# Performance work log

Measured on AMD Instinct MI355X. Metric: run time of the kernel, lower is better.

## Reference

```python
import jax, jax.numpy as jnp
import numpy as np

B, C, H, W = 16, 512, 64, 64
NH, HD = 8, 64  # num_heads, head_dim; C == NH*HD
EPS_ATTN = 1e-5
EPS_BN = 1e-5


def setup_inputs() -> dict:
    key = jax.random.key(0)
    k = jax.random.split(key, 9)
    x = jax.random.normal(k[0], (B, C, H, W), dtype=jnp.float32)
    # grouped 1x1 conv qkv: groups=NH, in/group=HD, out/group=3*HD
    w1 = jax.random.normal(k[1], (NH, 3 * HD, HD), dtype=jnp.float32) * 0.05
    b1 = jax.random.normal(k[2], (NH, 3 * HD), dtype=jnp.float32) * 0.01
    # grouped 1x1 conv qkv2: groups=HD, in/group=NH, out/group=3*NH
    w2 = jax.random.normal(k[3], (HD, 3 * NH, NH), dtype=jnp.float32) * 0.05
    b2 = jax.random.normal(k[4], (HD, 3 * NH), dtype=jnp.float32) * 0.01
    gamma = 1.0 + 0.1 * jax.random.normal(k[5], (C,), dtype=jnp.float32)
    beta = 0.1 * jax.random.normal(k[6], (C,), dtype=jnp.float32)
    rmean = 0.1 * jax.random.normal(k[7], (C,), dtype=jnp.float32)
    rvar = 0.5 + jax.random.uniform(k[8], (C,), dtype=jnp.float32)
    return {"x": x, "w1": w1, "b1": b1, "w2": w2, "b2": b2,
            "gamma": gamma, "beta": beta, "rmean": rmean, "rvar": rvar}


def _signed_sqrt_softmax(a):
    a = jnp.sign(a) * jnp.sqrt(jnp.abs(a) + EPS_ATTN)
    return jax.nn.softmax(a, axis=-1)


def reference(x, w1, b1, w2, b2, gamma, beta, rmean, rvar):
    N = H * W
    # ---- stage 1: grouped 1x1 conv (groups=NH) ----
    xg = x.reshape(B, NH, HD, N)
    qkv = jnp.einsum('goi,bgin->bgon', w1, xg) + b1[None, :, :, None]  # [B,NH,3HD,N]
    # torch grouped-conv channel order is group-major -> flatten then split as in source
    q, k, v = jnp.moveaxis(qkv.reshape(B, 3 * C, N).reshape(B, 3, NH, HD, N), 1, 0)
    attn = jnp.einsum('bhdn,bhen->bhde', q, k) * (HD ** -0.5)  # [B,NH,HD,HD]
    attn = _signed_sqrt_softmax(attn)
    out = jnp.einsum('bhde,bhen->bhdn', attn, v)  # [B,NH,HD,N]
    x1 = out.reshape(B, C, H, W) + x
    x1 = jnp.transpose(x1.reshape(B, NH, HD, H, W), (0, 2, 1, 3, 4)).reshape(B, C, H, W)
    # ---- BatchNorm2d (eval mode) + ReLU ----
    inv = gamma / jnp.sqrt(rvar + EPS_BN)
    y = x1 * inv[None, :, None, None] + (beta - rmean * inv)[None, :, None, None]
    xr = jnp.maximum(y, 0.0)
    # ---- stage 2: grouped 1x1 conv (groups=HD) ----
    xg2 = xr.reshape(B, HD, NH, N)
    qkv2 = jnp.einsum('goi,bgin->bgon', w2, xg2) + b2[None, :, :, None]  # [B,HD,3NH,N]
    q2, k2, v2 = jnp.moveaxis(qkv2.reshape(B, 3 * C, N).reshape(B, 3, HD, NH, N), 1, 0)
    attn2 = jnp.einsum('bdhn,bden->bdhe', q2, k2) * (NH ** -0.5)  # [B,HD,NH,NH]
    attn2 = _signed_sqrt_softmax(attn2)
    out2 = jnp.einsum('bdhe,bden->bdhn', attn2, v2)  # [B,HD,NH,N]
    x2 = jnp.transpose(out2.reshape(B, HD, NH, H, W), (0, 2, 1, 3, 4)).reshape(B, C, H, W) + y
    return x2
```

## Files before the change

### kernel.cpp

```cpp
#include <hip/hip_runtime.h>

#define N_ 4096

typedef __attribute__((ext_vector_type(8))) short bf16x8;
typedef __attribute__((ext_vector_type(4))) short bf16x4;
typedef __attribute__((ext_vector_type(4))) float f32x4;

__device__ __forceinline__ float ssqrt(float a) {
  if (a == 0.f) return 0.f;
  return copysignf(sqrtf(fabsf(a) + 1e-5f), a);
}

__device__ __forceinline__ ushort f2bf(float f) {
  uint u = __float_as_uint(f);
  u += 0x7fff + ((u >> 16) & 1);
  return (ushort)(u >> 16);
}
__device__ __forceinline__ float bf2f(ushort h) {
  return __uint_as_float((uint)h << 16);
}

__device__ __forceinline__ void split2(float f, ushort& hi, ushort& lo) {
  uint u = __float_as_uint(f);
  hi = (ushort)(u >> 16);
  float lof = f - __uint_as_float(u & 0xffff0000u);
  lo = (ushort)(__float_as_uint(lof) >> 16);
}

__device__ __forceinline__ f32x4 mfma16(bf16x8 a, bf16x8 b, f32x4 c) {
  return __builtin_amdgcn_mfma_f32_16x16x32_bf16(a, b, c, 0, 0, 0);
}

__device__ __forceinline__ bf16x8 relu8(bf16x8 v) {
  union { bf16x8 h; uint u[4]; } x;
  x.h = v;
#pragma unroll
  for (int i = 0; i < 4; ++i) {
    uint m = x.u[i] & 0x80008000u;
    x.u[i] &= ~((m >> 15) * 0xFFFFu);
  }
  return x.h;
}

__device__ __forceinline__ bf16x8 ld8_b64(const ushort* p) {
  bf16x4 a = *(const bf16x4*)p;
  bf16x4 b = *(const bf16x4*)(p + 4);
  return (bf16x8){a[0], a[1], a[2], a[3], b[0], b[1], b[2], b[3]};
}

__global__ __launch_bounds__(256) void k1_gram(const float* __restrict__ x,
    float* __restrict__ Gp, float* __restrict__ sums) {
  const int GQ[6] = {0, 0, 1, 1, 2, 2};
  const int GK[6] = {2, 3, 3, 4, 4, 5};
  int bid = (blockIdx.x & 7) * 48 + (blockIdx.x >> 3);
  int s = bid / 96, rem = bid % 96;
  int b = rem / 6, pid = rem % 6;
  int gq = GQ[pid], gk = GK[pid];
  const float* A = x + ((size_t)b * 512 + gq * 64) * N_ + s * 1024;
  const float* B = x + ((size_t)b * 512 + gk * 64) * N_ + s * 1024;
  __shared__ __attribute__((aligned(16))) ushort Ah[64][72], Al[64][72];
  __shared__ __attribute__((aligned(16))) ushort Bh[64][72], Bl[64][72];
  int t = threadIdx.x;
  int lr = t >> 2, lq = t & 3;
  int l = t & 63, w = t >> 6;
  int mw = (w >> 1) * 32, nw = (w & 1) * 32;
  int fr = l & 15, ko = (l >> 4) * 8;
  float sumA = 0.f, sumB = 0.f;
  f32x4 acc[2][2];
#pragma unroll
  for (int i = 0; i < 2; ++i)
#pragma unroll
    for (int j = 0; j < 2; ++j) acc[i][j] = (f32x4){0.f, 0.f, 0.f, 0.f};

  for (int kt = 0; kt < 16; ++kt) {
    int kbase = kt * 64 + lq * 16;
#pragma unroll
    for (int j = 0; j < 4; ++j) {
      float4 va = *(const float4*)(A + (size_t)lr * N_ + kbase + j * 4);
      float4 vb = *(const float4*)(B + (size_t)lr * N_ + kbase + j * 4);
      sumA += va.x + va.y + va.z + va.w;
      sumB += vb.x + vb.y + vb.z + vb.w;
      ushort4 ha, la, hb, lb;
      split2(va.x, ha.x, la.x); split2(va.y, ha.y, la.y);
      split2(va.z, ha.z, la.z); split2(va.w, ha.w, la.w);
      split2(vb.x, hb.x, lb.x); split2(vb.y, hb.y, lb.y);
      split2(vb.z, hb.z, lb.z); split2(vb.w, hb.w, lb.w);
      int c0 = lq * 16 + j * 4;
      *(ushort4*)&Ah[lr][c0] = ha;
      *(ushort4*)&Al[lr][c0] = la;
      *(ushort4*)&Bh[lr][c0] = hb;
      *(ushort4*)&Bl[lr][c0] = lb;
    }
    __syncthreads();
#pragma unroll
    for (int wk = 0; wk < 2; ++wk) {
      int kk = wk * 32 + ko;
      bf16x8 ah[2], al[2], bh[2], bl[2];
#pragma unroll
      for (int mt = 0; mt < 2; ++mt) {
        ah[mt] = *(const bf16x8*)&Ah[mw + mt * 16 + fr][kk];
        al[mt] = *(const bf16x8*)&Al[mw + mt * 16 + fr][kk];
      }
#pragma unroll
      for (int nt = 0; nt < 2; ++nt) {
        bh[nt] = *(const bf16x8*)&Bh[nw + nt * 16 + fr][kk];
        bl[nt] = *(const bf16x8*)&Bl[nw + nt * 16 + fr][kk];
      }
#pragma unroll
      for (int mt = 0; mt < 2; ++mt)
#pragma unroll
        for (int nt = 0; nt < 2; ++nt) {
          acc[mt][nt] = mfma16(ah[mt], bh[nt], acc[mt][nt]);
          acc[mt][nt] = mfma16(ah[mt], bl[nt], acc[mt][nt]);
          acc[mt][nt] = mfma16(al[mt], bh[nt], acc[mt][nt]);
        }
    }
    __syncthreads();
  }
  size_t base = ((size_t)s * 96 + rem) * 4096;
#pragma unroll
  for (int mt = 0; mt < 2; ++mt)
#pragma unroll
    for (int nt = 0; nt < 2; ++nt)
#pragma unroll
      for (int reg = 0; reg < 4; ++reg) {
        int gr = mw + mt * 16 + (l >> 4) * 4 + reg;
        int gc = nw + nt * 16 + fr;
        Gp[base + (size_t)gr * 64 + gc] = acc[mt][nt][reg];
      }
  sumA += __shfl_xor(sumA, 1); sumA += __shfl_xor(sumA, 2);
  sumB += __shfl_xor(sumB, 1); sumB += __shfl_xor(sumB, 2);
  if (lq == 0) {
    sums[(((size_t)s * 16 + b) * 6 + gq) * 64 + lr] = sumA;
    sums[(((size_t)s * 16 + b) * 6 + gk) * 64 + lr] = sumB;
  }
}

__global__ __launch_bounds__(256) void k2_attn1(
    const float* __restrict__ w1, const float* __restrict__ b1,
    const float* __restrict__ Gp, const float* __restrict__ sums,
    ushort* __restrict__ M1h, ushort* __restrict__ M1l,
    float* __restrict__ pbv1) {
  const int PID[8] = {0, 1, 1, 2, 3, 3, 4, 5};
  int bh = blockIdx.x;
  int b = bh >> 3, h = bh & 7;
  int pid = PID[h];
  int mq = h, mk = 8 + h, mv = 16 + h;
  int gq = mq / 3, oq0 = (mq % 3) * 64;
  int gk = mk / 3, ok0 = (mk % 3) * 64;
  int gv = mv / 3, ov0 = (mv % 3) * 64;
  __shared__ __attribute__((aligned(16))) float Gs[64][68];
  __shared__ __attribute__((aligned(16))) float Was[64][68];
  __shared__ __attribute__((aligned(16))) float Wbs[64][68];
  __shared__ __attribute__((aligned(16))) float Ts[64][68];
  __shared__ float sxs[64], sks[64], vqs[64], vks[64], bvs[64];
  int t = threadIdx.x, tx = t & 15, ty = t >> 4;
  int d0 = ty * 4, e0 = tx * 4;

  for (int f = t; f < 4096; f += 256) {
    int dd = f >> 6, ee = f & 63;
    float g = 0.f;
#pragma unroll
    for (int s = 0; s < 4; ++s)
      g += Gp[((size_t)s * 96 + b * 6 + pid) * 4096 + f];
    Gs[dd][ee] = g;
    Was[dd][ee] = w1[((size_t)(gq * 192 + oq0 + dd)) * 64 + ee];
    Wbs[dd][ee] = w1[((size_t)(gk * 192 + ok0 + dd)) * 64 + ee];
  }
  if (t < 64) {
    float v = 0.f, w = 0.f;
#pragma unroll
    for (int s = 0; s < 4; ++s) {
      v += sums[(((size_t)s * 16 + b) * 6 + gq) * 64 + t];
      w += sums[(((size_t)s * 16 + b) * 6 + gk) * 64 + t];
    }
    sxs[t] = v; sks[t] = w;
    bvs[t] = b1[gv * 192 + ov0 + t];
  }
  __syncthreads();
  if (t < 64) {
    float vq = 0.f, vk = 0.f;
    for (int i = 0; i < 64; ++i) { vq += Was[t][i] * sxs[i]; vk += Wbs[t][i] * sks[i]; }
    vqs[t] = vq; vks[t] = vk;
  }
  {
    float acc[4][4] = {};
    for (int i = 0; i < 64; i += 4) {
      float4 a4[4], g4[4];
#pragma unroll
      for (int r = 0; r < 4; ++r) a4[r] = *(const float4*)&Was[d0 + r][i];
#pragma unroll
      for (int k = 0; k < 4; ++k) g4[k] = *(const float4*)&Gs[i + k][e0];
#pragma unroll
      for (int r = 0; r < 4; ++r) {
        const float* ap = (const float*)&a4[r];
#pragma unroll
        for (int k = 0; k < 4; ++k) {
          const float* gp = (const float*)&g4[k];
#pragma unroll
          for (int c = 0; c < 4; ++c) acc[r][c] += ap[k] * gp[c];
        }
      }
    }
#pragma unroll
    for (int r = 0; r < 4; ++r)
#pragma unroll
      for (int c = 0; c < 4; ++c) Ts[d0 + r][e0 + c] = acc[r][c];
  }
  __syncthreads();
  float P[4][4];
  {
    float s[4][4] = {};
    for (int j = 0; j < 64; j += 4) {
      float4 t4[4], w4[4];
#pragma unroll
      for (int r = 0; r < 4; ++r) t4[r] = *(const float4*)&Ts[d0 + r][j];
#pragma unroll
      for (int c = 0; c < 4; ++c) w4[c] = *(const float4*)&Wbs[e0 + c][j];
#pragma unroll
      for (int r = 0; r < 4; ++r)
#pragma unroll
        for (int c = 0; c < 4; ++c)
          s[r][c] += t4[r].x * w4[c].x + t4[r].y * w4[c].y
                   + t4[r].z * w4[c].z + t4[r].w * w4[c].w;
    }
    float bq_[4], bk_[4];
#pragma unroll
    for (int r = 0; r < 4; ++r) bq_[r] = b1[gq * 192 + oq0 + d0 + r];
#pragma unroll
    for (int c = 0; c < 4; ++c) bk_[c] = b1[gk * 192 + ok0 + e0 + c];
#pragma unroll
    for (int r = 0; r < 4; ++r)
#pragma unroll
      for (int c = 0; c < 4; ++c) {
        float v = (s[r][c] + bq_[r] * vks[e0 + c] + bk_[c] * vqs[d0 + r]
                   + 4096.f * bq_[r] * bk_[c]) * 0.125f;
        s[r][c] = ssqrt(v);
      }
#pragma unroll
    for (int r = 0; r < 4; ++r) {
      float m = fmaxf(fmaxf(s[r][0], s[r][1]), fmaxf(s[r][2], s[r][3]));
#pragma unroll
      for (int mm = 1; mm < 16; mm <<= 1) m = fmaxf(m, __shfl_xor(m, mm));
      float sum = 0.f;
#pragma unroll
      for (int c = 0; c < 4; ++c) { s[r][c] = expf(s[r][c] - m); sum += s[r][c]; }
#pragma unroll
      for (int mm = 1; mm < 16; mm <<= 1) sum += __shfl_xor(sum, mm);
      float inv = 1.f / sum;
#pragma unroll
      for (int c = 0; c < 4; ++c) P[r][c] = s[r][c] * inv;
    }
  }
#pragma unroll
  for (int r = 0; r < 4; ++r)
#pragma unroll
    for (int c = 0; c < 4; ++c) Gs[d0 + r][e0 + c] = P[r][c];
  for (int f = t; f < 4096; f += 256) {
    int ee = f >> 6, ii = f & 63;
    Was[ee][ii] = w1[((size_t)(gv * 192 + ov0 + ee)) * 64 + ii];
  }
  __syncthreads();
  {
    float acc[4][4] = {};
    for (int e = 0; e < 64; e += 4) {
      float4 p4[4], v4[4];
#pragma unroll
      for (int r = 0; r < 4; ++r) p4[r] = *(const float4*)&Gs[d0 + r][e];
#pragma unroll
      for (int k = 0; k < 4; ++k) v4[k] = *(const float4*)&Was[e + k][e0];
#pragma unroll
      for (int r = 0; r < 4; ++r) {
        const float* pp = (const float*)&p4[r];
#pragma unroll
        for (int k = 0; k < 4; ++k) {
          const float* vp = (const float*)&v4[k];
#pragma unroll
          for (int c = 0; c < 4; ++c) acc[r][c] += pp[k] * vp[c];
        }
      }
    }
    ushort* MoH = M1h + (size_t)bh * 4096;
    ushort* MoL = M1l + (size_t)bh * 4096;
#pragma unroll
    for (int r = 0; r < 4; ++r)
#pragma unroll
      for (int c = 0; c < 4; ++c) {
        float vv = acc[r][c];
        ushort hi = f2bf(vv);
        MoH[(size_t)(d0 + r) * 64 + e0 + c] = hi;
        MoL[(size_t)(d0 + r) * 64 + e0 + c] = f2bf(vv - bf2f(hi));
      }
  }
  if (t < 64) {
    float pb = 0.f;
    for (int e = 0; e < 64; ++e) pb += Gs[t][e] * bvs[e];
    pbv1[(size_t)bh * 64 + t] = pb;
  }
}

__global__ __launch_bounds__(256) void k3_out1(const float* __restrict__ x,
    const ushort* __restrict__ M1h, const ushort* __restrict__ M1l,
    const float* __restrict__ pbv1,
    const float* __restrict__ gamma, const float* __restrict__ beta,
    const float* __restrict__ rmean, const float* __restrict__ rvar,
    ushort* __restrict__ y) {
  int orig = (blockIdx.x & 7) * 256 + (blockIdx.x >> 3);
  int b = orig >> 7;
  int rem = orig & 127;
  int chunk = rem >> 3, h = rem & 7;
  int bh = b * 8 + h;
  int gv = (16 + h) / 3;
  const float* Xv = x + ((size_t)b * 512 + gv * 64) * N_ + chunk * 256;
  const float* Xr = x + ((size_t)b * 512 + h * 64) * N_ + chunk * 256;
  ushort* Y = y + (size_t)b * 512 * N_ + chunk * 256;

  __shared__ __attribute__((aligned(16))) ushort Xth[64][68], Xtl[64][68];
  __shared__ float pbs[64], invs[64], adds[64];
  int t = threadIdx.x;
  if (t < 64) {
    pbs[t] = pbv1[(size_t)bh * 64 + t];
    int c = t * 8 + h;
    float iv = gamma[c] / sqrtf(rvar[c] + 1e-5f);
    invs[t] = iv;
    adds[t] = beta[c] - rmean[c] * iv;
  }
  int l = t & 63, w = t >> 6;
  int dq = w >> 1, nq = w & 1;
  int fr = l & 15, g = l >> 4;

  bf16x8 mh[2][2], ml[2][2];
  {
    const ushort* MbH = M1h + (size_t)bh * 4096;
    const ushort* MbL = M1l + (size_t)bh * 4096;
#pragma unroll
    for (int dr = 0; dr < 2; ++dr)
#pragma unroll
      for (int wk = 0; wk < 2; ++wk) {
        int off = (dq * 32 + dr * 16 + fr) * 64 + wk * 32 + g * 8;
        mh[dr][wk] = *(const bf16x8*)(MbH + off);
        ml[dr][wk] = *(const bf16x8*)(MbL + off);
      }
  }

  int e2 = t >> 3, q = t & 7;
  for (int tile = 0; tile < 4; ++tile) {
    int nb = tile * 64;
    {
      const float* r0p = Xv + (size_t)(2 * e2) * N_ + nb + q * 8;
      const float* r1p = r0p + N_;
      float4 a0 = *(const float4*)r0p, a1 = *(const float4*)(r0p + 4);
      float4 b0 = *(const float4*)r1p, b1 = *(const float4*)(r1p + 4);
      float ra[8] = {a0.x, a0.y, a0.z, a0.w, a1.x, a1.y, a1.z, a1.w};
      float rb[8] = {b0.x, b0.y, b0.z, b0.w, b1.x, b1.y, b1.z, b1.w};
#pragma unroll
      for (int i = 0; i < 8; ++i) {
        int n = q * 8 + i;
        ushort h0, l0, h1, l1;
        split2(ra[i], h0, l0);
        split2(rb[i], h1, l1);
        *(uint*)&Xth[n][2 * e2] = (uint)h0 | ((uint)h1 << 16);
        *(uint*)&Xtl[n][2 * e2] = (uint)l0 | ((uint)l1 << 16);
      }
    }
    __syncthreads();
    f32x4 acc[2][2];
#pragma unroll
    for (int i = 0; i < 2; ++i)
#pragma unroll
      for (int j = 0; j < 2; ++j) acc[i][j] = (f32x4){0.f, 0.f, 0.f, 0.f};
#pragma unroll
    for (int wk = 0; wk < 2; ++wk) {
      int kk = wk * 32 + g * 8;
      bf16x8 xh[2], xl[2];
#pragma unroll
      for (int nr = 0; nr < 2; ++nr) {
        xh[nr] = ld8_b64(&Xth[nq * 32 + nr * 16 + fr][kk]);
        xl[nr] = ld8_b64(&Xtl[nq * 32 + nr * 16 + fr][kk]);
      }
#pragma unroll
      for (int nr = 0; nr < 2; ++nr)
#pragma unroll
        for (int dr = 0; dr < 2; ++dr) {
          acc[nr][dr] = mfma16(xh[nr], mh[dr][wk], acc[nr][dr]);
          acc[nr][dr] = mfma16(xh[nr], ml[dr][wk], acc[nr][dr]);
          acc[nr][dr] = mfma16(xl[nr], mh[dr][wk], acc[nr][dr]);
        }
    }
#pragma unroll
    for (int nr = 0; nr < 2; ++nr)
#pragma unroll
      for (int dr = 0; dr < 2; ++dr) {
        int d = dq * 32 + dr * 16 + fr;
        int n0 = nb + nq * 32 + nr * 16 + g * 4;
        float4 rx = *(const float4*)(Xr + (size_t)d * N_ + n0);
        float iv = invs[d], ad = adds[d], pb = pbs[d];
        float4 v;
        v.x = (acc[nr][dr][0] + pb + rx.x) * iv + ad;
        v.y = (acc[nr][dr][1] + pb + rx.y) * iv + ad;
        v.z = (acc[nr][dr][2] + pb + rx.z) * iv + ad;
        v.w = (acc[nr][dr][3] + pb + rx.w) * iv + ad;
        ushort4 o;
        o.x = f2bf(v.x); o.y = f2bf(v.y); o.z = f2bf(v.z); o.w = f2bf(v.w);
        *(ushort4*)(Y + (size_t)(d * 8 + h) * N_ + n0) = o;
      }
    __syncthreads();
  }
}

__global__ __launch_bounds__(256) void k46_stage2(const ushort* __restrict__ y,
    const float* __restrict__ w2, const float* __restrict__ b2,
    float* __restrict__ out) {
  int orig = (blockIdx.x & 7) * 128 + (blockIdx.x >> 3);
  int b = orig >> 6, d = orig & 63;
  int gq = d / 3, gk = (64 + d) / 3, gv = (128 + d) / 3;
  int mq = d, mk = 64 + d, mv = 128 + d;
  int g2q = mq / 3, oq0 = (mq % 3) * 8;
  int g2k = mk / 3, ok0 = (mk % 3) * 8;
  int g2v = mv / 3, ov0 = (mv % 3) * 8;
  const ushort* Aq = y + ((size_t)b * 512 + gq * 8) * N_;
  const ushort* Ak = y + ((size_t)b * 512 + gk * 8) * N_;
  int t = threadIdx.x;
  int l = t & 63, w = t >> 6;

  __shared__ float W2q[8][8], W2k[8][8], W2v[8][8];
  __shared__ float bq2[8], bk2[8], bv2[8];
  __shared__ float red[4][16][16];
  __shared__ float gbuf[80];
  __shared__ float Ps[8][9];
  __shared__ float Msh[8][8], pbsh[8];
  if (t < 64) {
    int hh = t >> 3, ee = t & 7;
    W2q[hh][ee] = w2[(size_t)(g2q * 24 + oq0 + hh) * 8 + ee];
    W2k[hh][ee] = w2[(size_t)(g2k * 24 + ok0 + hh) * 8 + ee];
    W2v[hh][ee] = w2[(size_t)(g2v * 24 + ov0 + hh) * 8 + ee];
  }
  if (t < 8) {
    bq2[t] = b2[g2q * 24 + oq0 + t];
    bk2[t] = b2[g2k * 24 + ok0 + t];
    bv2[t] = b2[g2v * 24 + ov0 + t];
  }

  {
    int row16 = l & 15;
    int ko = (l >> 4) * 8;
    const ushort* Arow = (row16 < 8) ? (Aq + (size_t)row16 * N_)
                                     : (Ak + (size_t)(row16 - 8) * N_);
    const ushort* Brow = (row16 < 8) ? (Ak + (size_t)row16 * N_) : nullptr;
    ushort bv = (row16 == 8) ? (ushort)0x3F80 : (ushort)0;
    bf16x8 bconst = {(short)bv, (short)bv, (short)bv, (short)bv,
                     (short)bv, (short)bv, (short)bv, (short)bv};
    f32x4 accA = (f32x4){0.f, 0.f, 0.f, 0.f};
    f32x4 accB = (f32x4){0.f, 0.f, 0.f, 0.f};
    int nbase = w * 1024 + ko;
#pragma unroll 4
    for (int step = 0; step < 16; ++step) {
      int n0 = nbase + step * 32;
      int n1 = n0 + 512;
      bf16x8 a0 = relu8(*(const bf16x8*)(Arow + n0));
      bf16x8 a1 = relu8(*(const bf16x8*)(Arow + n1));
      bf16x8 b0, b1;
      if (row16 < 8) {
        b0 = relu8(*(const bf16x8*)(Brow + n0));
        b1 = relu8(*(const bf16x8*)(Brow + n1));
      } else {
        b0 = bconst; b1 = bconst;
      }
      accA = mfma16(a0, b0, accA);
      accB = mfma16(a1, b1, accB);
    }
    f32x4 acc;
#pragma unroll
    for (int r = 0; r < 4; ++r) acc[r] = accA[r] + accB[r];
#pragma unroll
    for (int r = 0; r < 4; ++r) red[w][(l >> 4) * 4 + r][l & 15] = acc[r];
  }
  __syncthreads();
  {
    int rr = t >> 4, cc = t & 15;
    float csum = red[0][rr][cc] + red[1][rr][cc] + red[2][rr][cc] + red[3][rr][cc];
    if (rr < 8 && cc < 8) gbuf[rr * 8 + cc] = csum;
    else if (cc == 8) gbuf[rr < 8 ? 64 + rr : 72 + (rr - 8)] = csum;
  }
  __syncthreads();

  if (t < 64) {
    int hh = t >> 3, ee = t & 7;
    float s = 0.f;
#pragma unroll
    for (int i = 0; i < 8; ++i) {
      float pg = 0.f;
#pragma unroll
      for (int j = 0; j < 8; ++j) pg += gbuf[i * 8 + j] * W2k[ee][j];
      s += W2q[hh][i] * pg;
    }
    float dq = 0.f, dk = 0.f;
#pragma unroll
    for (int i = 0; i < 8; ++i) { dq += W2q[hh][i] * gbuf[64 + i]; dk += W2k[ee][i] * gbuf[72 + i]; }
    s = (s + bq2[hh] * dk + bk2[ee] * dq + 4096.f * bq2[hh] * bk2[ee]) * 0.35355339059327373f;
    s = ssqrt(s);
    float m = s;
#pragma unroll
    for (int mm = 1; mm < 8; mm <<= 1) m = fmaxf(m, __shfl_xor(m, mm));
    float p = expf(s - m);
    float sum = p;
#pragma unroll
    for (int mm = 1; mm < 8; mm <<= 1) sum += __shfl_xor(sum, mm);
    p /= sum;
    Ps[t >> 3][t & 7] = p;
  }
  __syncthreads();
  if (t < 64) {
    int hh = t >> 3, ee = t & 7;
    float mo = 0.f;
#pragma unroll
    for (int e = 0; e < 8; ++e) mo += Ps[hh][e] * W2v[e][ee];
    Msh[hh][ee] = mo;
  }
  if (t < 8) {
    float pb = 0.f;
#pragma unroll
    for (int e = 0; e < 8; ++e) pb += Ps[t][e] * bv2[e];
    pbsh[t] = pb;
  }
  __syncthreads();

  float msr[8][8], pbr[8];
#pragma unroll
  for (int hh = 0; hh < 8; ++hh) {
    pbr[hh] = pbsh[hh];
#pragma unroll
    for (int i = 0; i < 8; ++i) msr[hh][i] = Msh[hh][i];
  }
  const ushort* Yv = y + ((size_t)b * 512 + gv * 8) * N_;
  const ushort* Yr = y + ((size_t)b * 512 + d) * N_;
  float* O = out + ((size_t)b * 512 + d) * N_;
  for (int it = 0; it < 4; ++it) {
    int n4 = (it * 256 + t) * 4;
    float xv0[8], xv1[8], xv2[8], xv3[8];
#pragma unroll
    for (int i = 0; i < 8; ++i) {
      ushort4 u = *(const ushort4*)(Yv + (size_t)i * N_ + n4);
      xv0[i] = fmaxf(bf2f(u.x), 0.f); xv1[i] = fmaxf(bf2f(u.y), 0.f);
      xv2[i] = fmaxf(bf2f(u.z), 0.f); xv3[i] = fmaxf(bf2f(u.w), 0.f);
    }
#pragma unroll
    for (int hh = 0; hh < 8; ++hh) {
      float4 a;
      a.x = pbr[hh]; a.y = pbr[hh]; a.z = pbr[hh]; a.w = pbr[hh];
#pragma unroll
      for (int i = 0; i < 8; ++i) {
        float m = msr[hh][i];
        a.x += m * xv0[i]; a.y += m * xv1[i];
        a.z += m * xv2[i]; a.w += m * xv3[i];
      }
      ushort4 r = *(const ushort4*)(Yr + (size_t)hh * 64 * N_ + n4);
      a.x += bf2f(r.x); a.y += bf2f(r.y); a.z += bf2f(r.z); a.w += bf2f(r.w);
      *(float4*)(O + (size_t)hh * 64 * N_ + n4) = a;
    }
  }
}

extern "C" void kernel_launch(void* const* d_in, const int* in_sizes, int n_in,
                              void* d_out, int out_size, void* d_ws, size_t ws_size,
                              hipStream_t stream) {
  const float* x     = (const float*)d_in[0];
  const float* w1    = (const float*)d_in[1];
  const float* b1    = (const float*)d_in[2];
  const float* w2    = (const float*)d_in[3];
  const float* b2    = (const float*)d_in[4];
  const float* gamma = (const float*)d_in[5];
  const float* beta  = (const float*)d_in[6];
  const float* rmean = (const float*)d_in[7];
  const float* rvar  = (const float*)d_in[8];
  float* out = (float*)d_out;

  ushort* y    = (ushort*)d_ws;
  float* Gp    = (float*)(y + 33554432);
  float* sums  = Gp + 1572864;
  ushort* M1h  = (ushort*)(sums + 24576);
  ushort* M1l  = M1h + 524288;
  float* pbv1  = (float*)(M1l + 524288);
  size_t need = (size_t)67108864 + 6291456 + 98304 + 2097152 + 32768;
  if (ws_size < need) return;

  k1_gram<<<384, 256, 0, stream>>>(x, Gp, sums);
  k2_attn1<<<128, 256, 0, stream>>>(w1, b1, Gp, sums, M1h, M1l, pbv1);
  k3_out1<<<2048, 256, 0, stream>>>(x, M1h, M1l, pbv1, gamma, beta, rmean, rvar, y);
  k46_stage2<<<1024, 256, 0, stream>>>(y, w2, b2, out);
}
```

Before: 167.0 us.

## Prefetch V and residual tiles before softmax and double-buffer output loop

Issues the global loads for the first V and residual tile before the small attention/softmax computation, so their latency overlaps that work. The output loop then prefetches the next iteration's tiles into registers while computing the current one. The 8x8 mixing matrix is now read from shared memory as float4 on each use instead of being held in 72 registers, trading register pressure for extra LDS reads. The added prefetch buffers also raise register use, which could reduce occupancy.

```diff
diff --git a/kernel.cpp b/kernel.cpp
--- a/kernel.cpp
+++ b/kernel.cpp
@@ -428,7 +428,8 @@
   __shared__ float red[4][16][16];
   __shared__ float gbuf[80];
   __shared__ float Ps[8][9];
-  __shared__ float Msh[8][8], pbsh[8];
+  __shared__ __attribute__((aligned(16))) float Msh[8][8];
+  __shared__ float pbsh[8];
   if (t < 64) {
     int hh = t >> 3, ee = t & 7;
     W2q[hh][ee] = w2[(size_t)(g2q * 24 + oq0 + hh) * 8 + ee];
@@ -484,6 +485,19 @@
   }
   __syncthreads();
 
+  const ushort* Yv = y + ((size_t)b * 512 + gv * 8) * N_;
+  const ushort* Yr = y + ((size_t)b * 512 + d) * N_;
+  float* O = out + ((size_t)b * 512 + d) * N_;
+  ushort4 vbuf[8], rbuf[8];
+  {
+    int n4 = t * 4;
+#pragma unroll
+    for (int i = 0; i < 8; ++i) {
+      vbuf[i] = *(const ushort4*)(Yv + (size_t)i * N_ + n4);
+      rbuf[i] = *(const ushort4*)(Yr + (size_t)i * 64 * N_ + n4);
+    }
+  }
+
   if (t < 64) {
     int hh = t >> 3, ee = t & 7;
     float s = 0.f;
@@ -525,38 +539,45 @@
   }
   __syncthreads();
 
-  float msr[8][8], pbr[8];
-#pragma unroll
-  for (int hh = 0; hh < 8; ++hh) {
-    pbr[hh] = pbsh[hh];
-#pragma unroll
-    for (int i = 0; i < 8; ++i) msr[hh][i] = Msh[hh][i];
-  }
-  const ushort* Yv = y + ((size_t)b * 512 + gv * 8) * N_;
-  const ushort* Yr = y + ((size_t)b * 512 + d) * N_;
-  float* O = out + ((size_t)b * 512 + d) * N_;
   for (int it = 0; it < 4; ++it) {
+    ushort4 vnext[8], rnext[8];
+    if (it < 3) {
+      int n4n = ((it + 1) * 256 + t) * 4;
+#pragma unroll
+      for (int i = 0; i < 8; ++i) {
+        vnext[i] = *(const ushort4*)(Yv + (size_t)i * N_ + n4n);
+        rnext[i] = *(const ushort4*)(Yr + (size_t)i * 64 * N_ + n4n);
+      }
+    }
     int n4 = (it * 256 + t) * 4;
     float xv0[8], xv1[8], xv2[8], xv3[8];
 #pragma unroll
     for (int i = 0; i < 8; ++i) {
-      ushort4 u = *(const ushort4*)(Yv + (size_t)i * N_ + n4);
+      ushort4 u = vbuf[i];
       xv0[i] = fmaxf(bf2f(u.x), 0.f); xv1[i] = fmaxf(bf2f(u.y), 0.f);
       xv2[i] = fmaxf(bf2f(u.z), 0.f); xv3[i] = fmaxf(bf2f(u.w), 0.f);
     }
 #pragma unroll
     for (int hh = 0; hh < 8; ++hh) {
+      float4 m0 = *(const float4*)&Msh[hh][0];
+      float4 m1 = *(const float4*)&Msh[hh][4];
+      float mr[8] = {m0.x, m0.y, m0.z, m0.w, m1.x, m1.y, m1.z, m1.w};
+      float pb = pbsh[hh];
       float4 a;
-      a.x = pbr[hh]; a.y = pbr[hh]; a.z = pbr[hh]; a.w = pbr[hh];
+      a.x = pb; a.y = pb; a.z = pb; a.w = pb;
 #pragma unroll
       for (int i = 0; i < 8; ++i) {
-        float m = msr[hh][i];
+        float m = mr[i];
         a.x += m * xv0[i]; a.y += m * xv1[i];
         a.z += m * xv2[i]; a.w += m * xv3[i];
       }
-      ushort4 r = *(const ushort4*)(Yr + (size_t)hh * 64 * N_ + n4);
+      ushort4 r = rbuf[hh];
       a.x += bf2f(r.x); a.y += bf2f(r.y); a.z += bf2f(r.z); a.w += bf2f(r.w);
       *(float4*)(O + (size_t)hh * 64 * N_ + n4) = a;
+    }
+    if (it < 3) {
+#pragma unroll
+      for (int i = 0; i < 8; ++i) { vbuf[i] = vnext[i]; rbuf[i] = rnext[i]; }
     }
   }
 }
```

New measurement: 182.1 us. 9.0% more time.
